# Kernel optimization log

Hardware: AMD Instinct MI355X
Metric: run time of the kernel (lower is better)

The kernel has to match this reference:

```python
import jax, jax.numpy as jnp
import numpy as np

IN_F, OUT_F, GROUP = 4096, 11008, 128
N_GROUPS = IN_F // GROUP  # 32 (in_features divisible by group_size -> no padding)


def setup_inputs() -> dict:
    key = jax.random.key(0)
    kx, kw, ks, kb = jax.random.split(key, 4)
    x = jax.random.normal(kx, (4, 2048, IN_F), dtype=jnp.float32)
    weight_q = jax.random.randint(kw, (OUT_F, IN_F), -128, 128, dtype=jnp.int32).astype(jnp.int8)
    scales = jax.random.uniform(ks, (OUT_F, N_GROUPS), dtype=jnp.float32) * 0.01 + 1e-4
    bias = jax.random.normal(kb, (OUT_F,), dtype=jnp.float32)
    return {"x": x, "weight_q": weight_q, "scales": scales, "bias": bias}


def reference(x, weight_q, scales, bias):
    # Dequantize: group-wise scale along in_features, cast to fp16 (as torch .half())
    W = (weight_q.astype(jnp.float32).reshape(OUT_F, N_GROUPS, GROUP)
         * scales[:, :, None]).reshape(OUT_F, IN_F).astype(jnp.float16)
    # fp16 linear: y = x W^T + b, then back to fp32
    y = jnp.einsum('bsi,oi->bso', x.astype(jnp.float16), W) + bias.astype(jnp.float16)
    return y.astype(jnp.float32)
```

## Files before the change

kernel.cpp:

```cpp
#include <hip/hip_runtime.h>

#define IN_F 4096
#define OUT_F 11008
#define NGROUPS 32
#define M_TOTAL 8192
#define BM 256
#define BN 256
#define BK 64
#define NKT (IN_F / BK)

typedef _Float16 half_t;
typedef __attribute__((ext_vector_type(8))) _Float16 half8;
typedef __attribute__((ext_vector_type(4))) _Float16 half4v;
typedef __attribute__((ext_vector_type(4))) float f32x4;
typedef __attribute__((ext_vector_type(4))) int i32x4;

typedef __attribute__((address_space(1))) const void gvoid_t;
typedef __attribute__((address_space(3))) void lvoid_t;

__global__ void convert_x_k(const float* __restrict__ x, half_t* __restrict__ xh) {
  const int n4 = M_TOTAL * IN_F / 4;
  int stride = gridDim.x * blockDim.x;
  for (int i = blockIdx.x * blockDim.x + threadIdx.x; i < n4; i += stride) {
    f32x4 v = __builtin_nontemporal_load((const f32x4*)x + i);
    half4v h;
    h[0] = (_Float16)v[0]; h[1] = (_Float16)v[1];
    h[2] = (_Float16)v[2]; h[3] = (_Float16)v[3];
    ((half4v*)xh)[i] = h;
  }
}

__global__ void dequant_w_k(const int* __restrict__ wq,
                            const float* __restrict__ scales,
                            half_t* __restrict__ wh) {
  int row = blockIdx.x;
  int t = threadIdx.x;
  size_t base = (size_t)row * IN_F + (size_t)t * 8;
  float s = scales[row * NGROUPS + (t >> 4)];
  i32x4 q0 = __builtin_nontemporal_load((const i32x4*)(wq + base));
  i32x4 q1 = __builtin_nontemporal_load((const i32x4*)(wq + base) + 1);
  half8 h;
#pragma unroll
  for (int j = 0; j < 4; ++j) h[j] = (_Float16)((float)q0[j] * s);
#pragma unroll
  for (int j = 0; j < 4; ++j) h[4 + j] = (_Float16)((float)q1[j] * s);
  *(half8*)(wh + base) = h;
}


__device__ __forceinline__ void rd4(half8 (&d)[4], const char* base) {
#pragma unroll
  for (int i = 0; i < 4; ++i) d[i] = *(const half8*)(base + i * 1024);
}

__device__ __forceinline__ void mfma16(f32x4 (&acc)[8][4], const half8 (&a)[4],
                                       const half8 (&b)[4], int mh) {
#pragma unroll
  for (int i = 0; i < 4; ++i)
#pragma unroll
    for (int j = 0; j < 4; ++j)
      acc[mh * 4 + i][j] =
          __builtin_amdgcn_mfma_f32_16x16x32_f16(a[i], b[j], acc[mh * 4 + i][j], 0, 0, 0);
}

#define BAR() __builtin_amdgcn_s_barrier()
#define SB0() __builtin_amdgcn_sched_barrier(0)
#define PRIO1() __builtin_amdgcn_s_setprio(1)
#define PRIO0() __builtin_amdgcn_s_setprio(0)
#define VMCNT(N) asm volatile("s_waitcnt vmcnt(" #N ")" ::: "memory")
#define LGKM(N) asm volatile("s_waitcnt lgkmcnt(" #N ")" ::: "memory")

#define STAGE(OP, KH, KT, S)                                                          \
  do {                                                                                \
    const half_t* g_ = ((OP) ? pBsrc : pAsrc) + (KT) * 64 + (KH) * 32;                \
    char* d_ = (char*)&lds[S][OP][KH][0] + wvoff;                                     \
    __builtin_amdgcn_global_load_lds((gvoid_t*)g_, (lvoid_t*)d_, 16, 0, 0);           \
    __builtin_amdgcn_global_load_lds((gvoid_t*)(g_ + 128 * IN_F),                     \
                                     (lvoid_t*)(d_ + 8192), 16, 0, 0);                \
  } while (0)

__global__ __launch_bounds__(512, 2) void gemm_k(const half_t* __restrict__ A,
                                                 const half_t* __restrict__ B,
                                                 const float* __restrict__ bias,
                                                 float* __restrict__ C) {
  __shared__ __align__(16) half_t lds[2][2][2][8192];

  const int tid = threadIdx.x;
  const int lane = tid & 63;
  const int wv = tid >> 6;
  const int wm = wv >> 2;
  const int wn = wv & 3;
  const int wvoff = wv << 10;

  const int nwg = gridDim.x;
  const int perx = nwg >> 3;
  const int L = ((int)blockIdx.x & 7) * perx + ((int)blockIdx.x >> 3);
  const int band = L >> 7;
  const int rr_ = L & 127;
  const int bn0 = band << 2;
  const int cols = (43 - bn0) < 4 ? (43 - bn0) : 4;
  const int bm = rr_ / cols;
  const int bn = bn0 + rr_ % cols;
  const int row0 = bm * BM;
  const int col0 = bn * BN;

  const int c16 = (tid & 3) * 16;
  const int srow = tid >> 2;
  const int clog = c16 ^ ((srow & 6) << 3);
  const int kidx = clog >> 1;
  const half_t* pAsrc = A + (size_t)(row0 + srow) * IN_F + kidx;
  const half_t* pBsrc = B + (size_t)(col0 + srow) * IN_F + kidx;

  const int r16 = lane & 15;
  const int kg = lane >> 4;
  const int arow = wm * 128 + r16;
  const int brow = wn * 64 + r16;
  const int aoff = arow * 64 + ((kg * 16) ^ ((arow & 6) << 3));
  const int boff = brow * 64 + ((kg * 16) ^ ((brow & 6) << 3));

  f32x4 acc[8][4];
#pragma unroll
  for (int m = 0; m < 8; ++m)
#pragma unroll
    for (int n = 0; n < 4; ++n) acc[m][n] = (f32x4){0.f, 0.f, 0.f, 0.f};

  STAGE(0, 0, 0, 0);
  STAGE(1, 0, 0, 0);
  STAGE(0, 1, 0, 0);
  STAGE(1, 1, 0, 0);
  STAGE(0, 0, 1, 1);
  STAGE(1, 0, 1, 1);
  VMCNT(8);
  BAR();
  SB0();

  half8 aR0[4], aR1[4], bR0[4], bR1[4];
  rd4(aR0, (const char*)&lds[0][0][0][0] + aoff);
  rd4(bR0, (const char*)&lds[0][1][0][0] + boff);

  for (int t = 0; t < NKT - 2; ++t) {
    const int s = t & 1, ns = s ^ 1;
    const char* Ab0 = (const char*)&lds[s][0][0][0];
    const char* Bb0 = (const char*)&lds[s][1][0][0];
    const char* Ab1 = (const char*)&lds[s][0][1][0];
    const char* Bb1 = (const char*)&lds[s][1][1][0];
    const char* Ab0n = (const char*)&lds[ns][0][0][0];
    const char* Bb0n = (const char*)&lds[ns][1][0][0];
    rd4(aR1, Ab0 + aoff + 4096);
    STAGE(0, 1, t + 1, ns);
    LGKM(4); SB0(); PRIO1();
    mfma16(acc, aR0, bR0, 0);
    PRIO0(); VMCNT(6); BAR(); SB0();
    rd4(aR0, Ab1 + aoff);
    rd4(bR1, Bb1 + boff);
    STAGE(1, 1, t + 1, ns);
    LGKM(8); SB0(); PRIO1();
    mfma16(acc, aR1, bR0, 1);
    PRIO0(); VMCNT(6); BAR(); SB0();
    rd4(aR1, Ab1 + aoff + 4096);
    STAGE(0, 0, t + 2, s);
    LGKM(4); SB0(); PRIO1();
    mfma16(acc, aR0, bR1, 0);
    PRIO0(); VMCNT(6); BAR(); SB0();
    rd4(aR0, Ab0n + aoff);
    rd4(bR0, Bb0n + boff);
    STAGE(1, 0, t + 2, s);
    LGKM(8); SB0(); PRIO1();
    mfma16(acc, aR1, bR1, 1);
    PRIO0(); VMCNT(6); BAR(); SB0();
  }

  {
    const char* Ab0 = (const char*)&lds[0][0][0][0];
    const char* Bb0 = (const char*)&lds[0][1][0][0];
    const char* Ab1 = (const char*)&lds[0][0][1][0];
    const char* Bb1 = (const char*)&lds[0][1][1][0];
    const char* Ab0n = (const char*)&lds[1][0][0][0];
    const char* Bb0n = (const char*)&lds[1][1][0][0];
    rd4(aR1, Ab0 + aoff + 4096);
    STAGE(0, 1, 63, 1);
    LGKM(4); SB0(); PRIO1();
    mfma16(acc, aR0, bR0, 0);
    PRIO0(); VMCNT(6); BAR(); SB0();
    rd4(aR0, Ab1 + aoff);
    rd4(bR1, Bb1 + boff);
    STAGE(1, 1, 63, 1);
    LGKM(8); SB0(); PRIO1();
    mfma16(acc, aR1, bR0, 1);
    PRIO0(); VMCNT(6); BAR(); SB0();
    rd4(aR1, Ab1 + aoff + 4096);
    LGKM(4); SB0(); PRIO1();
    mfma16(acc, aR0, bR1, 0);
    PRIO0(); VMCNT(4); BAR(); SB0();
    rd4(aR0, Ab0n + aoff);
    rd4(bR0, Bb0n + boff);
    LGKM(8); SB0(); PRIO1();
    mfma16(acc, aR1, bR1, 1);
    PRIO0(); VMCNT(0); BAR(); SB0();
  }
  {
    const char* Ab0 = (const char*)&lds[1][0][0][0];
    const char* Ab1 = (const char*)&lds[1][0][1][0];
    const char* Bb1 = (const char*)&lds[1][1][1][0];
    rd4(aR1, Ab0 + aoff + 4096);
    LGKM(4); SB0();
    mfma16(acc, aR0, bR0, 0);
    rd4(aR0, Ab1 + aoff);
    rd4(bR1, Bb1 + boff);
    LGKM(8); SB0();
    mfma16(acc, aR1, bR0, 1);
    rd4(aR1, Ab1 + aoff + 4096);
    LGKM(4); SB0();
    mfma16(acc, aR0, bR1, 0);
    LGKM(0); SB0();
    mfma16(acc, aR1, bR1, 1);
  }

  const int kg4 = kg * 4;
#pragma unroll
  for (int nf = 0; nf < 4; ++nf) {
    int col = col0 + wn * 64 + nf * 16 + r16;
    _Float16 bh = (_Float16)bias[col];
#pragma unroll
    for (int mf = 0; mf < 8; ++mf) {
      int rb = row0 + wm * 128 + mf * 16 + kg4;
#pragma unroll
      for (int r = 0; r < 4; ++r) {
        _Float16 v = (_Float16)acc[mf][nf][r] + bh;
        __builtin_nontemporal_store((float)v, &C[(size_t)(rb + r) * OUT_F + col]);
      }
    }
  }
}

__global__ void naive_k(const float* __restrict__ x, const int* __restrict__ wq,
                        const float* __restrict__ scales, const float* __restrict__ bias,
                        float* __restrict__ out) {
  long idx = (long)blockIdx.x * blockDim.x + threadIdx.x;
  if (idx >= (long)M_TOTAL * OUT_F) return;
  int m = (int)(idx / OUT_F);
  int n = (int)(idx % OUT_F);
  float acc = 0.f;
  for (int g = 0; g < NGROUPS; ++g) {
    float s = scales[n * NGROUPS + g];
    for (int k = g * 128; k < (g + 1) * 128; ++k) {
      _Float16 xv = (_Float16)x[(size_t)m * IN_F + k];
      _Float16 wv = (_Float16)((float)wq[(size_t)n * IN_F + k] * s);
      acc += (float)xv * (float)wv;
    }
  }
  _Float16 r = (_Float16)acc + (_Float16)bias[n];
  out[idx] = (float)r;
}

extern "C" void kernel_launch(void* const* d_in, const int* in_sizes, int n_in,
                              void* d_out, int out_size, void* d_ws, size_t ws_size,
                              hipStream_t stream) {
  const float* x = (const float*)d_in[0];
  const int* wq = (const int*)d_in[1];
  const float* scales = (const float*)d_in[2];
  const float* bias = (const float*)d_in[3];
  float* out = (float*)d_out;

  const size_t xh_bytes = (size_t)M_TOTAL * IN_F * sizeof(half_t);
  const size_t wh_bytes = (size_t)OUT_F * IN_F * sizeof(half_t);

  if (ws_size >= xh_bytes + wh_bytes) {
    half_t* xh = (half_t*)d_ws;
    half_t* wh = (half_t*)((char*)d_ws + xh_bytes);
    convert_x_k<<<2048, 256, 0, stream>>>(x, xh);
    dequant_w_k<<<OUT_F, 512, 0, stream>>>(wq, scales, wh);
    gemm_k<<<(M_TOTAL / BM) * (OUT_F / BN), 512, 0, stream>>>(xh, wh, bias, out);
  } else {
    long total = (long)M_TOTAL * OUT_F;
    naive_k<<<(int)((total + 255) / 256), 256, 0, stream>>>(x, wq, scales, bias, out);
  }
}
```

Before: 754.5 us.

## Restructure GEMM main loop into eight-phase schedule with single register set

Replaces the register double-buffered main loop (aR0/aR1/bR0/bR1 with overlapped LDS reads) with an 8-phase macro-driven schedule that uses a single A/B register set and waits on all LDS reads (lgkmcnt(0)) before each MFMA block, adding an extra barrier per phase. Launch bounds drop from two waves-per-EU occupancy target to one, and the prologue prefetches one more stage. The aim is to cut register pressure and make the pipeline more regular. In exchange it loses LDS-read/MFMA overlap within a wave, adds barriers, and halves occupancy.

```diff
diff --git a/kernel.cpp b/kernel.cpp
--- a/kernel.cpp
+++ b/kernel.cpp
@@ -79,7 +79,32 @@
                                      (lvoid_t*)(d_ + 8192), 16, 0, 0);                \
   } while (0)
 
-__global__ __launch_bounds__(512, 2) void gemm_k(const half_t* __restrict__ A,
+#define PH(SL, KH, MH, RB, SOP, SKH, SKT, SSL, FENCE)                  \
+  do {                                                                 \
+    rd4(a, (const char*)&lds[SL][0][KH][0] + aoff + (MH) * 4096);      \
+    if (RB) rd4(b, (const char*)&lds[SL][1][KH][0] + boff);            \
+    STAGE(SOP, SKH, SKT, SSL);                                         \
+    SB0(); BAR();                                                      \
+    LGKM(0); SB0(); PRIO1();                                           \
+    mfma16(acc, a, b, MH);                                             \
+    PRIO0();                                                           \
+    if (FENCE) VMCNT(6);                                               \
+    BAR(); SB0();                                                      \
+  } while (0)
+
+#define PHN(SL, KH, MH, RB, FENCE)                                     \
+  do {                                                                 \
+    rd4(a, (const char*)&lds[SL][0][KH][0] + aoff + (MH) * 4096);      \
+    if (RB) rd4(b, (const char*)&lds[SL][1][KH][0] + boff);            \
+    SB0(); BAR();                                                      \
+    LGKM(0); SB0(); PRIO1();                                           \
+    mfma16(acc, a, b, MH);                                             \
+    PRIO0();                                                           \
+    if (FENCE) VMCNT(0);                                               \
+    BAR(); SB0();                                                      \
+  } while (0)
+
+__global__ __launch_bounds__(512, 1) void gemm_k(const half_t* __restrict__ A,
                                                  const half_t* __restrict__ B,
                                                  const float* __restrict__ bias,
                                                  float* __restrict__ C) {
@@ -130,90 +155,32 @@
   STAGE(1, 1, 0, 0);
   STAGE(0, 0, 1, 1);
   STAGE(1, 0, 1, 1);
-  VMCNT(8);
+  STAGE(1, 1, 1, 1);
+  VMCNT(6);
   BAR();
   SB0();
 
-  half8 aR0[4], aR1[4], bR0[4], bR1[4];
-  rd4(aR0, (const char*)&lds[0][0][0][0] + aoff);
-  rd4(bR0, (const char*)&lds[0][1][0][0] + boff);
-
-  for (int t = 0; t < NKT - 2; ++t) {
-    const int s = t & 1, ns = s ^ 1;
-    const char* Ab0 = (const char*)&lds[s][0][0][0];
-    const char* Bb0 = (const char*)&lds[s][1][0][0];
-    const char* Ab1 = (const char*)&lds[s][0][1][0];
-    const char* Bb1 = (const char*)&lds[s][1][1][0];
-    const char* Ab0n = (const char*)&lds[ns][0][0][0];
-    const char* Bb0n = (const char*)&lds[ns][1][0][0];
-    rd4(aR1, Ab0 + aoff + 4096);
-    STAGE(0, 1, t + 1, ns);
-    LGKM(4); SB0(); PRIO1();
-    mfma16(acc, aR0, bR0, 0);
-    PRIO0(); VMCNT(6); BAR(); SB0();
-    rd4(aR0, Ab1 + aoff);
-    rd4(bR1, Bb1 + boff);
-    STAGE(1, 1, t + 1, ns);
-    LGKM(8); SB0(); PRIO1();
-    mfma16(acc, aR1, bR0, 1);
-    PRIO0(); VMCNT(6); BAR(); SB0();
-    rd4(aR1, Ab1 + aoff + 4096);
-    STAGE(0, 0, t + 2, s);
-    LGKM(4); SB0(); PRIO1();
-    mfma16(acc, aR0, bR1, 0);
-    PRIO0(); VMCNT(6); BAR(); SB0();
-    rd4(aR0, Ab0n + aoff);
-    rd4(bR0, Bb0n + boff);
-    STAGE(1, 0, t + 2, s);
-    LGKM(8); SB0(); PRIO1();
-    mfma16(acc, aR1, bR1, 1);
-    PRIO0(); VMCNT(6); BAR(); SB0();
-  }
-
+  half8 a[4], b[4];
+  for (int u = 0; u < 31; ++u) {
+    const int t1 = 2 * u + 1, n0 = 2 * u + 2, n1 = 2 * u + 3;
+    PH(0, 0, 0, 1, 0, 1, t1, 1, 0);
+    PH(0, 0, 1, 0, 1, 0, n0, 0, 0);
+    PH(0, 1, 0, 1, 0, 0, n0, 0, 0);
+    PH(0, 1, 1, 0, 1, 1, n0, 0, 1);
+    PH(1, 0, 0, 1, 0, 1, n0, 0, 0);
+    PH(1, 0, 1, 0, 1, 0, n1, 1, 0);
+    PH(1, 1, 0, 1, 0, 0, n1, 1, 0);
+    PH(1, 1, 1, 0, 1, 1, n1, 1, 1);
+  }
   {
-    const char* Ab0 = (const char*)&lds[0][0][0][0];
-    const char* Bb0 = (const char*)&lds[0][1][0][0];
-    const char* Ab1 = (const char*)&lds[0][0][1][0];
-    const char* Bb1 = (const char*)&lds[0][1][1][0];
-    const char* Ab0n = (const char*)&lds[1][0][0][0];
-    const char* Bb0n = (const char*)&lds[1][1][0][0];
-    rd4(aR1, Ab0 + aoff + 4096);
-    STAGE(0, 1, 63, 1);
-    LGKM(4); SB0(); PRIO1();
-    mfma16(acc, aR0, bR0, 0);
-    PRIO0(); VMCNT(6); BAR(); SB0();
-    rd4(aR0, Ab1 + aoff);
-    rd4(bR1, Bb1 + boff);
-    STAGE(1, 1, 63, 1);
-    LGKM(8); SB0(); PRIO1();
-    mfma16(acc, aR1, bR0, 1);
-    PRIO0(); VMCNT(6); BAR(); SB0();
-    rd4(aR1, Ab1 + aoff + 4096);
-    LGKM(4); SB0(); PRIO1();
-    mfma16(acc, aR0, bR1, 0);
-    PRIO0(); VMCNT(4); BAR(); SB0();
-    rd4(aR0, Ab0n + aoff);
-    rd4(bR0, Bb0n + boff);
-    LGKM(8); SB0(); PRIO1();
-    mfma16(acc, aR1, bR1, 1);
-    PRIO0(); VMCNT(0); BAR(); SB0();
-  }
-  {
-    const char* Ab0 = (const char*)&lds[1][0][0][0];
-    const char* Ab1 = (const char*)&lds[1][0][1][0];
-    const char* Bb1 = (const char*)&lds[1][1][1][0];
-    rd4(aR1, Ab0 + aoff + 4096);
-    LGKM(4); SB0();
-    mfma16(acc, aR0, bR0, 0);
-    rd4(aR0, Ab1 + aoff);
-    rd4(bR1, Bb1 + boff);
-    LGKM(8); SB0();
-    mfma16(acc, aR1, bR0, 1);
-    rd4(aR1, Ab1 + aoff + 4096);
-    LGKM(4); SB0();
-    mfma16(acc, aR0, bR1, 0);
-    LGKM(0); SB0();
-    mfma16(acc, aR1, bR1, 1);
+    PH(0, 0, 0, 1, 0, 1, 63, 1, 0);
+    PHN(0, 0, 1, 0, 0);
+    PHN(0, 1, 0, 1, 0);
+    PHN(0, 1, 1, 0, 2);
+    PHN(1, 0, 0, 1, 0);
+    PHN(1, 0, 1, 0, 0);
+    PHN(1, 1, 0, 1, 0);
+    PHN(1, 1, 1, 0, 0);
   }
 
   const int kg4 = kg * 4;
```

New measurement: 775.5 us. 1.03x slower.
